# Kernel tuning notes

Hardware: AMD Instinct MI355X
Metric: run time of the kernel (lower is better)

## Reference

```python
import jax, jax.numpy as jnp
import numpy as np
from jax import lax

WEIGHT_REG = 1e-06
BIAS_REG = 1e-06
DROP_REG = 1e-05
EPS = 1e-07
TEMP = 0.1


def setup_inputs() -> dict:
    key = jax.random.key(0)
    ks = jax.random.split(key, 9)
    B, T, D, H = 256, 512, 128, 128
    x = jax.random.normal(ks[0], (B, T, D), dtype=jnp.float32)
    # 0.05 scale keeps LSTM gates out of deep saturation
    weight_ih = jax.random.normal(ks[1], (4 * H, D), dtype=jnp.float32) * 0.05
    weight_hh = jax.random.normal(ks[2], (4 * H, H), dtype=jnp.float32) * 0.05
    bias_ih = jax.random.normal(ks[3], (4 * H,), dtype=jnp.float32) * 0.05
    bias_hh = jax.random.normal(ks[4], (4 * H,), dtype=jnp.float32) * 0.05
    p_logit = jax.random.normal(ks[5], (1,), dtype=jnp.float32)
    p_logit_rec = jax.random.normal(ks[6], (1,), dtype=jnp.float32)
    unif_x = jax.random.uniform(ks[7], (B, D), dtype=jnp.float32)
    unif_h = jax.random.uniform(ks[8], (B, H), dtype=jnp.float32)
    return {"x": x, "weight_ih": weight_ih, "weight_hh": weight_hh,
            "bias_ih": bias_ih, "bias_hh": bias_hh,
            "p_logit": p_logit, "p_logit_rec": p_logit_rec,
            "unif_x": unif_x, "unif_h": unif_h}


def _concrete_mask(u, p):
    # random_tensor = 1 - sigmoid((logit(p) + logit(u)) / temp)
    logit = (jnp.log(p + EPS) - jnp.log(1.0 - p + EPS)
             + jnp.log(u + EPS) - jnp.log(1.0 - u + EPS))
    return 1.0 - jax.nn.sigmoid(logit / TEMP)


def reference(x, weight_ih, weight_hh, bias_ih, bias_hh,
              p_logit, p_logit_rec, unif_x, unif_h):
    B, T, D = x.shape
    H = weight_hh.shape[1]
    p = jax.nn.sigmoid(p_logit)        # [1]
    p_rec = jax.nn.sigmoid(p_logit_rec)  # [1]

    # masks are sampled once (at t=0) and reused every timestep
    mask_x = _concrete_mask(unif_x, p)      # [B, D]
    mask_h = _concrete_mask(unif_h, p_rec)  # [B, H]

    x_d = x * mask_x[:, None, :] / (1.0 - p)  # dropout on input, all steps

    h0 = jnp.zeros((B, H), dtype=x.dtype)
    c0 = jnp.zeros((B, H), dtype=x.dtype)

    def step(carry, xt):
        h, c = carry
        hd = h * mask_h / (1.0 - p_rec)  # recurrent concrete dropout
        gates = xt @ weight_ih.T + bias_ih + hd @ weight_hh.T + bias_hh
        i_g, f_g, g_g, o_g = jnp.split(gates, 4, axis=-1)  # torch LSTMCell order
        c_new = jax.nn.sigmoid(f_g) * c + jax.nn.sigmoid(i_g) * jnp.tanh(g_g)
        h_new = jax.nn.sigmoid(o_g) * jnp.tanh(c_new)
        return (h_new, c_new), h_new

    (h_last, _), hs = lax.scan(step, (h0, c0), jnp.swapaxes(x_d, 0, 1))
    x_out = jnp.swapaxes(hs, 0, 1)  # [B, T, H]

    sum_kernel = jnp.sum(weight_ih ** 2)
    sum_rec = jnp.sum(weight_hh ** 2)
    sum_bias = jnp.sum(bias_ih ** 2) + jnp.sum(bias_hh ** 2)
    weights_reg = WEIGHT_REG * (sum_kernel / (1.0 - p) + sum_rec / (1.0 - p_rec))
    bias_reg = BIAS_REG * sum_bias
    ent_k = p * jnp.log(p) + (1.0 - p) * jnp.log(1.0 - p)
    ent_r = p_rec * jnp.log(p_rec) + (1.0 - p_rec) * jnp.log(1.0 - p_rec)
    drop_reg = DROP_REG * (D * ent_k + H * ent_r)
    regularization = weights_reg + bias_reg + drop_reg  # [1]

    return (x_out, h_last, regularization, p, p_rec)
```

## Files before the change

### kernel.cpp

```cpp
#include <hip/hip_runtime.h>
#include <cstddef>

#define NB 256
#define NT 512
#define ND 128
#define NH 128
#define NG 512
#define NM (NB * NT)

constexpr float F_EPS  = 1e-7f;
constexpr float F_TEMP = 0.1f;

typedef _Float16 h2_t __attribute__((ext_vector_type(2)));
typedef _Float16 h4_t __attribute__((ext_vector_type(4)));
typedef _Float16 h8_t __attribute__((ext_vector_type(8)));
typedef float    fx4  __attribute__((ext_vector_type(4)));

#if defined(__has_builtin)
#  if __has_builtin(__builtin_amdgcn_fdot2)
#    define FDOT2(a, b, c) __builtin_amdgcn_fdot2((a), (b), (c), false)
#  endif
#endif
#ifndef FDOT2
#  define FDOT2(a, b, c) ((c) + (float)(a)[0] * (float)(b)[0] + (float)(a)[1] * (float)(b)[1])
#endif

__device__ __forceinline__ float fexp2(float x) {
#if defined(__has_builtin)
#  if __has_builtin(__builtin_amdgcn_exp2f)
    return __builtin_amdgcn_exp2f(x);
#  else
    return exp2f(x);
#  endif
#else
    return exp2f(x);
#endif
}
__device__ __forceinline__ float frcp(float x) {
#if defined(__has_builtin)
#  if __has_builtin(__builtin_amdgcn_rcpf)
    return __builtin_amdgcn_rcpf(x);
#  else
    return 1.0f / x;
#  endif
#else
    return 1.0f / x;
#endif
}
__device__ __forceinline__ float fsig(float x) {
    return frcp(1.0f + fexp2(x * -1.44269504088896f));
}
__device__ __forceinline__ float ftanh(float x) {
    return 1.0f - 2.0f * frcp(1.0f + fexp2(x * 2.88539008177793f));
}
__device__ __forceinline__ float sig(float x) { return 1.0f / (1.0f + expf(-x)); }

__device__ __forceinline__ void bar_lds() {
    asm volatile("s_waitcnt lgkmcnt(0)" ::: "memory");
    __builtin_amdgcn_sched_barrier(0);
    __builtin_amdgcn_s_barrier();
}

__global__ __launch_bounds__(256) void k_convert(const float* __restrict__ wih,
        const float* __restrict__ whh, _Float16* __restrict__ wih_h,
        _Float16* __restrict__ whh_h, float* __restrict__ partial) {
    int i = blockIdx.x * 256 + threadIdx.x;
    float4 a = ((const float4*)wih)[i];
    float4 b = ((const float4*)whh)[i];
    h4_t ah, bh;
    ah[0] = (_Float16)a.x; ah[1] = (_Float16)a.y; ah[2] = (_Float16)a.z; ah[3] = (_Float16)a.w;
    bh[0] = (_Float16)b.x; bh[1] = (_Float16)b.y; bh[2] = (_Float16)b.z; bh[3] = (_Float16)b.w;
    *(h4_t*)(wih_h + 4 * (size_t)i) = ah;
    *(h4_t*)(whh_h + 4 * (size_t)i) = bh;
    float sk = a.x * a.x + a.y * a.y + a.z * a.z + a.w * a.w;
    float sr = b.x * b.x + b.y * b.y + b.z * b.z + b.w * b.w;
    for (int off = 32; off; off >>= 1) {
        sk += __shfl_down(sk, off);
        sr += __shfl_down(sr, off);
    }
    if ((threadIdx.x & 63) == 0) {
        atomicAdd(partial + 0, sk);
        atomicAdd(partial + 1, sr);
    }
}

__global__ void k_tail(const float* __restrict__ bih, const float* __restrict__ bhh,
                       const float* __restrict__ pl, const float* __restrict__ plr,
                       const float* __restrict__ partial, float* __restrict__ out_tail) {
    __shared__ float red[8];
    int t = threadIdx.x;
    float v = bih[t], w2 = bhh[t];
    float sb = v * v + w2 * w2;
    for (int off = 32; off; off >>= 1) sb += __shfl_down(sb, off);
    int wid = t >> 6, lane = t & 63;
    if (lane == 0) red[wid] = sb;
    __syncthreads();
    if (t == 0) {
        float SB = 0.f;
        for (int i = 0; i < 8; i++) SB += red[i];
        float SK = partial[0], SR = partial[1];
        float p  = sig(pl[0]);
        float pr = sig(plr[0]);
        float wr = 1e-6f * (SK / (1.f - p) + SR / (1.f - pr));
        float br = 1e-6f * SB;
        float ek = p * logf(p) + (1.f - p) * logf(1.f - p);
        float er = pr * logf(pr) + (1.f - pr) * logf(1.f - pr);
        float dr = 1e-5f * ((float)ND * ek + (float)NH * er);
        out_tail[0] = wr + br + dr;
        out_tail[1] = p;
        out_tail[2] = pr;
    }
}

__global__ __launch_bounds__(256, 2) void k_gemm(const float* __restrict__ x,
        const _Float16* __restrict__ wih_h, const float* __restrict__ bih,
        const float* __restrict__ bhh, const float* __restrict__ pl,
        const float* __restrict__ unif_x, _Float16* __restrict__ Gp) {
    __shared__ _Float16 Alds[128 * 128];
    __shared__ _Float16 Wlds[128 * 128];
    __shared__ float sx[128];
    __shared__ float bsum[128];
    int t  = threadIdx.x;
    int m0 = blockIdx.x * 128;
    int j0 = blockIdx.y * 128;
    int b  = m0 >> 9;

    float p = sig(pl[0]);
    if (t < 128) {
        float u  = unif_x[b * ND + t];
        float lg = logf(p + F_EPS) - logf(1.f - p + F_EPS)
                 + logf(u + F_EPS) - logf(1.f - u + F_EPS);
        float mk = 1.f - sig(lg / F_TEMP);
        sx[t] = mk / (1.f - p);
    } else {
        int j = t - 128;
        bsum[j] = bih[j0 + j] + bhh[j0 + j];
    }
    __syncthreads();

#pragma unroll
    for (int i = 0; i < 8; i++) {
        int s   = i * 256 + t;
        int row = s >> 4;
        int s16 = s & 15;
        const float4* xp = (const float4*)(x + (size_t)(m0 + row) * ND + s16 * 8);
        float4 v0 = xp[0], v1 = xp[1];
        float4 s0 = *(const float4*)(sx + s16 * 8);
        float4 s1 = *(const float4*)(sx + s16 * 8 + 4);
        h8_t hv;
        hv[0] = (_Float16)(v0.x * s0.x); hv[1] = (_Float16)(v0.y * s0.y);
        hv[2] = (_Float16)(v0.z * s0.z); hv[3] = (_Float16)(v0.w * s0.w);
        hv[4] = (_Float16)(v1.x * s1.x); hv[5] = (_Float16)(v1.y * s1.y);
        hv[6] = (_Float16)(v1.z * s1.z); hv[7] = (_Float16)(v1.w * s1.w);
        *(h8_t*)(&Alds[(size_t)row * 128 + ((s16 ^ (row & 7)) << 3)]) = hv;
        h8_t wv = *(const h8_t*)(wih_h + (size_t)(j0 + row) * ND + s16 * 8);
        *(h8_t*)(&Wlds[(size_t)row * 128 + ((s16 ^ (row & 7)) << 3)]) = wv;
    }
    __syncthreads();

    int w  = t >> 6, l = t & 63;
    int lr = l & 15, lg = l >> 4;
    fx4 acc[2][8] = {};
#pragma unroll
    for (int kk = 0; kk < 4; kk++) {
        h8_t af[2], bf[8];
#pragma unroll
        for (int mt = 0; mt < 2; mt++) {
            int r = 32 * w + 16 * mt + lr;
            af[mt] = *(const h8_t*)(&Alds[(size_t)r * 128 + (((4 * kk + lg) ^ (r & 7)) << 3)]);
        }
#pragma unroll
        for (int nt = 0; nt < 8; nt++) {
            int r = 16 * nt + lr;
            bf[nt] = *(const h8_t*)(&Wlds[(size_t)r * 128 + (((4 * kk + lg) ^ (r & 7)) << 3)]);
        }
#pragma unroll
        for (int mt = 0; mt < 2; mt++)
#pragma unroll
            for (int nt = 0; nt < 8; nt++)
                acc[mt][nt] = __builtin_amdgcn_mfma_f32_16x16x32_f16(af[mt], bf[nt], acc[mt][nt], 0, 0, 0);
    }

#pragma unroll
    for (int mt = 0; mt < 2; mt++)
#pragma unroll
        for (int nt = 0; nt < 8; nt++) {
            int j = j0 + 16 * nt + lr;
            int m = m0 + 32 * w + 16 * mt + 4 * lg;
            float bv = bsum[16 * nt + lr];
            h4_t o;
#pragma unroll
            for (int q = 0; q < 4; q++) o[q] = (_Float16)(acc[mt][nt][q] + bv);
            *(h4_t*)(Gp + (size_t)j * NM + m) = o;
        }
}

__global__ __launch_bounds__(512, 2) void k_lstm(const _Float16* __restrict__ Gp,
        const _Float16* __restrict__ whh_h, const float* __restrict__ plr,
        const float* __restrict__ unif_h,
        float* __restrict__ xout, float* __restrict__ hlast) {
    __shared__ _Float16 hd[128];
    __shared__ float gates[512];
    int b = blockIdx.x;
    int j = threadIdx.x;
    int gate = j >> 7;

    h2_t w[64];
    {
        const _Float16* wr = whh_h + (size_t)j * NH;
#pragma unroll
        for (int i = 0; i < 16; i++) {
            h8_t a = *(const h8_t*)(wr + 8 * i);
#pragma unroll
            for (int q = 0; q < 4; q++)
                w[4 * i + q] = (h2_t){a[2 * q], a[2 * q + 1]};
        }
    }

    float pr = sig(plr[0]);
    float h = 0.f, c = 0.f, msk = 0.f;
    if (j < 128) {
        float u  = unif_h[b * NH + j];
        float lg = logf(pr + F_EPS) - logf(1.f - pr + F_EPS)
                 + logf(u + F_EPS) - logf(1.f - u + F_EPS);
        float mk = 1.f - sig(lg / F_TEMP);
        msk = mk / (1.f - pr);
        hd[j] = (_Float16)0.f;
    }

    const _Float16* gp = Gp + (size_t)j * NM + (size_t)b * NT;
    float* xo = xout + (size_t)b * NT * NH + j;

    h8_t gcur = *(const h8_t*)(gp);
    __syncthreads();

    for (int w8 = 0; w8 < NT / 8; w8++) {
        h8_t gnx = gcur;
        if (w8 + 1 < NT / 8) gnx = *(const h8_t*)(gp + 8 * (w8 + 1));
#pragma unroll
        for (int e = 0; e < 8; e++) {
            float a0 = 0.f, a1 = 0.f, a2 = 0.f, a3 = 0.f;
#pragma unroll
            for (int i = 0; i < 16; i++) {
                h8_t hv = *(const h8_t*)(&hd[8 * i]);
                a0 = FDOT2(((h2_t){hv[0], hv[1]}), w[4 * i + 0], a0);
                a1 = FDOT2(((h2_t){hv[2], hv[3]}), w[4 * i + 1], a1);
                a2 = FDOT2(((h2_t){hv[4], hv[5]}), w[4 * i + 2], a2);
                a3 = FDOT2(((h2_t){hv[6], hv[7]}), w[4 * i + 3], a3);
            }
            float s = (float)gcur[e] + ((a0 + a1) + (a2 + a3));
            gates[j] = (gate == 2) ? ftanh(s) : fsig(s);
            bar_lds();
            if (j < 128) {
                float ig = gates[j],       fg = gates[j + 128];
                float gg = gates[j + 256], og = gates[j + 384];
                c = fg * c + ig * gg;
                h = og * ftanh(c);
                hd[j] = (_Float16)(h * msk);
                xo[(size_t)(8 * w8 + e) * NH] = h;
            }
            bar_lds();
        }
        gcur = gnx;
    }
    if (j < 128) hlast[(size_t)b * NH + j] = h;
}

extern "C" void kernel_launch(void* const* d_in, const int* in_sizes, int n_in,
                              void* d_out, int out_size, void* d_ws, size_t ws_size,
                              hipStream_t stream) {
    const float* x   = (const float*)d_in[0];
    const float* wih = (const float*)d_in[1];
    const float* whh = (const float*)d_in[2];
    const float* bih = (const float*)d_in[3];
    const float* bhh = (const float*)d_in[4];
    const float* pl  = (const float*)d_in[5];
    const float* plr = (const float*)d_in[6];
    const float* ux  = (const float*)d_in[7];
    const float* uh  = (const float*)d_in[8];

    float* out   = (float*)d_out;
    float* xout  = out;
    float* hlast = out + (size_t)NB * NT * NH;
    float* tail  = hlast + (size_t)NB * NH;

    _Float16* G     = (_Float16*)d_ws;
    _Float16* wih_h = (_Float16*)((char*)d_ws + (size_t)NG * NM * 2);
    _Float16* whh_h = wih_h + (size_t)NG * ND;
    float*    partial = (float*)(whh_h + (size_t)NG * NH);

    hipMemsetAsync(partial, 0, 2 * sizeof(float), stream);

    k_convert<<<64, 256, 0, stream>>>(wih, whh, wih_h, whh_h, partial);

    dim3 gg(NM / 128, NG / 128);
    k_gemm<<<gg, 256, 0, stream>>>(x, wih_h, bih, bhh, pl, ux, G);

    k_tail<<<1, 512, 0, stream>>>(bih, bhh, pl, plr, partial, tail);

    k_lstm<<<NB, 512, 0, stream>>>(G, whh_h, plr, uh, xout, hlast);
}
```

Before: 372.5 us.

## Split LSTM recurrent dot product across two thread halves per gate

New measurement: 393.7 us. +5.7%, slower.

```diff
diff --git a/kernel.cpp b/kernel.cpp
--- a/kernel.cpp
+++ b/kernel.cpp
@@ -195,21 +195,22 @@
         }
 }
 
-__global__ __launch_bounds__(512, 2) void k_lstm(const _Float16* __restrict__ Gp,
+__global__ __launch_bounds__(1024, 4) void k_lstm(const _Float16* __restrict__ Gp,
         const _Float16* __restrict__ whh_h, const float* __restrict__ plr,
         const float* __restrict__ unif_h,
         float* __restrict__ xout, float* __restrict__ hlast) {
     __shared__ _Float16 hd[128];
-    __shared__ float gates[512];
-    int b = blockIdx.x;
-    int j = threadIdx.x;
-    int gate = j >> 7;
-
-    h2_t w[64];
+    __shared__ float part[1024];
+    int b    = blockIdx.x;
+    int tid  = threadIdx.x;
+    int j    = tid & 511;
+    int half = tid >> 9;
+
+    h2_t w[32];
     {
-        const _Float16* wr = whh_h + (size_t)j * NH;
-#pragma unroll
-        for (int i = 0; i < 16; i++) {
+        const _Float16* wr = whh_h + (size_t)j * NH + 64 * half;
+#pragma unroll
+        for (int i = 0; i < 8; i++) {
             h8_t a = *(const h8_t*)(wr + 8 * i);
 #pragma unroll
             for (int q = 0; q < 4; q++)
@@ -219,51 +220,61 @@
 
     float pr = sig(plr[0]);
     float h = 0.f, c = 0.f, msk = 0.f;
-    if (j < 128) {
-        float u  = unif_h[b * NH + j];
+    if (tid < 128) {
+        float u  = unif_h[b * NH + tid];
         float lg = logf(pr + F_EPS) - logf(1.f - pr + F_EPS)
                  + logf(u + F_EPS) - logf(1.f - u + F_EPS);
         float mk = 1.f - sig(lg / F_TEMP);
         msk = mk / (1.f - pr);
-        hd[j] = (_Float16)0.f;
+        hd[tid] = (_Float16)0.f;
     }
 
     const _Float16* gp = Gp + (size_t)j * NM + (size_t)b * NT;
-    float* xo = xout + (size_t)b * NT * NH + j;
-
-    h8_t gcur = *(const h8_t*)(gp);
+    float* xo = xout + (size_t)b * NT * NH + tid;
+
+    h8_t gcur;
+#pragma unroll
+    for (int e = 0; e < 8; e++) gcur[e] = (_Float16)0.f;
+    if (half == 0) gcur = *(const h8_t*)(gp);
     __syncthreads();
 
     for (int w8 = 0; w8 < NT / 8; w8++) {
+#pragma unroll
+        for (int i = 0; i < 32; i++) asm volatile("" : "+v"(w[i]));
         h8_t gnx = gcur;
-        if (w8 + 1 < NT / 8) gnx = *(const h8_t*)(gp + 8 * (w8 + 1));
+        if (half == 0 && w8 + 1 < NT / 8)
+            gnx = *(const h8_t*)(gp + 8 * (w8 + 1));
+        const _Float16* hb = &hd[64 * half];
 #pragma unroll
         for (int e = 0; e < 8; e++) {
             float a0 = 0.f, a1 = 0.f, a2 = 0.f, a3 = 0.f;
 #pragma unroll
-            for (int i = 0; i < 16; i++) {
-                h8_t hv = *(const h8_t*)(&hd[8 * i]);
+            for (int i = 0; i < 8; i++) {
+                h8_t hv = *(const h8_t*)(hb + 8 * i);
                 a0 = FDOT2(((h2_t){hv[0], hv[1]}), w[4 * i + 0], a0);
                 a1 = FDOT2(((h2_t){hv[2], hv[3]}), w[4 * i + 1], a1);
                 a2 = FDOT2(((h2_t){hv[4], hv[5]}), w[4 * i + 2], a2);
                 a3 = FDOT2(((h2_t){hv[6], hv[7]}), w[4 * i + 3], a3);
             }
-            float s = (float)gcur[e] + ((a0 + a1) + (a2 + a3));
-            gates[j] = (gate == 2) ? ftanh(s) : fsig(s);
+            part[tid] = (float)gcur[e] + ((a0 + a1) + (a2 + a3));
             bar_lds();
-            if (j < 128) {
-                float ig = gates[j],       fg = gates[j + 128];
-                float gg = gates[j + 256], og = gates[j + 384];
+            if (tid < 128) {
+                float si = part[tid]       + part[tid + 512];
+                float sf = part[tid + 128] + part[tid + 640];
+                float sg = part[tid + 256] + part[tid + 768];
+                float so = part[tid + 384] + part[tid + 896];
+                float ig = fsig(si), fg = fsig(sf);
+                float gg = ftanh(sg), og = fsig(so);
                 c = fg * c + ig * gg;
                 h = og * ftanh(c);
-                hd[j] = (_Float16)(h * msk);
+                hd[tid] = (_Float16)(h * msk);
                 xo[(size_t)(8 * w8 + e) * NH] = h;
             }
             bar_lds();
         }
         gcur = gnx;
     }
-    if (j < 128) hlast[(size_t)b * NH + j] = h;
+    if (tid < 128) hlast[(size_t)b * NH + tid] = h;
 }
 
 extern "C" void kernel_launch(void* const* d_in, const int* in_sizes, int n_in,
@@ -298,5 +309,5 @@
 
     k_tail<<<1, 512, 0, stream>>>(bih, bhh, pl, plr, partial, tail);
 
-    k_lstm<<<NB, 512, 0, stream>>>(G, whh_h, plr, uh, xout, hlast);
-}
+    k_lstm<<<NB, 1024, 0, stream>>>(G, whh_h, plr, uh, xout, hlast);
+}
```

## Exchange LSTM gates via wave shuffles with double-buffered hidden state, one barrier

Applied to the files above, without the earlier changes.

Result: slower. 419.6 us (+12.6%).

```diff
diff --git a/kernel.cpp b/kernel.cpp
--- a/kernel.cpp
+++ b/kernel.cpp
@@ -7,6 +7,7 @@
 #define NH 128
 #define NG 512
 #define NM (NB * NT)
+#define NMP (NM + 64)
 
 constexpr float F_EPS  = 1e-7f;
 constexpr float F_TEMP = 0.1f;
@@ -47,11 +48,8 @@
     return 1.0f / x;
 #endif
 }
-__device__ __forceinline__ float fsig(float x) {
-    return frcp(1.0f + fexp2(x * -1.44269504088896f));
-}
 __device__ __forceinline__ float ftanh(float x) {
-    return 1.0f - 2.0f * frcp(1.0f + fexp2(x * 2.88539008177793f));
+    return 1.0f - 2.0f * frcp(1.0f + fexp2(x * 2.885390081777927f));
 }
 __device__ __forceinline__ float sig(float x) { return 1.0f / (1.0f + expf(-x)); }
 
@@ -191,19 +189,22 @@
             h4_t o;
 #pragma unroll
             for (int q = 0; q < 4; q++) o[q] = (_Float16)(acc[mt][nt][q] + bv);
-            *(h4_t*)(Gp + (size_t)j * NM + m) = o;
-        }
-}
-
-__global__ __launch_bounds__(512, 2) void k_lstm(const _Float16* __restrict__ Gp,
+            *(h4_t*)(Gp + (size_t)j * NMP + m) = o;
+        }
+}
+
+__global__ __launch_bounds__(512, 1) void k_lstm(const _Float16* __restrict__ Gp,
         const _Float16* __restrict__ whh_h, const float* __restrict__ plr,
         const float* __restrict__ unif_h,
         float* __restrict__ xout, float* __restrict__ hlast) {
-    __shared__ _Float16 hd[128];
-    __shared__ float gates[512];
-    int b = blockIdx.x;
-    int j = threadIdx.x;
-    int gate = j >> 7;
+    __shared__ _Float16 hd[2][128];
+    int b   = blockIdx.x;
+    int tid = threadIdx.x;
+    int l   = tid & 63;
+    int wv  = tid >> 6;
+    int n   = wv * 16 + (l & 15);
+    int g   = (l >> 4) & 3;
+    int j   = g * 128 + n;
 
     h2_t w[64];
     {
@@ -218,52 +219,65 @@
     }
 
     float pr = sig(plr[0]);
-    float h = 0.f, c = 0.f, msk = 0.f;
-    if (j < 128) {
-        float u  = unif_h[b * NH + j];
+    float msk;
+    {
+        float u  = unif_h[b * NH + n];
         float lg = logf(pr + F_EPS) - logf(1.f - pr + F_EPS)
                  + logf(u + F_EPS) - logf(1.f - u + F_EPS);
         float mk = 1.f - sig(lg / F_TEMP);
         msk = mk / (1.f - pr);
-        hd[j] = (_Float16)0.f;
-    }
-
-    const _Float16* gp = Gp + (size_t)j * NM + (size_t)b * NT;
-    float* xo = xout + (size_t)b * NT * NH + j;
+    }
+    float h = 0.f, c = 0.f;
+    if (g == 0) hd[0][n] = (_Float16)0.f;
+
+    const float k1 = (g == 2) ?  2.885390081777927f : -1.44269504088896f;
+    const float Ac = (g == 2) ? -2.f : 1.f;
+    const float Bc = (g == 2) ?  1.f : 0.f;
+
+    const _Float16* gp = Gp + (size_t)j * NMP + (size_t)b * NT;
+    float* xo = xout + (size_t)b * NT * NH + n;
 
     h8_t gcur = *(const h8_t*)(gp);
     __syncthreads();
 
     for (int w8 = 0; w8 < NT / 8; w8++) {
+#pragma unroll
+        for (int i = 0; i < 64; i++) asm volatile("" : "+v"(w[i]));
         h8_t gnx = gcur;
-        if (w8 + 1 < NT / 8) gnx = *(const h8_t*)(gp + 8 * (w8 + 1));
+        if (w8 + 1 < NT / 8)
+            gnx = *(const h8_t*)(gp + 8 * (w8 + 1));
 #pragma unroll
         for (int e = 0; e < 8; e++) {
+            const _Float16* hb = &hd[e & 1][0];
             float a0 = 0.f, a1 = 0.f, a2 = 0.f, a3 = 0.f;
 #pragma unroll
             for (int i = 0; i < 16; i++) {
-                h8_t hv = *(const h8_t*)(&hd[8 * i]);
+                h8_t hv = *(const h8_t*)(hb + 8 * i);
                 a0 = FDOT2(((h2_t){hv[0], hv[1]}), w[4 * i + 0], a0);
                 a1 = FDOT2(((h2_t){hv[2], hv[3]}), w[4 * i + 1], a1);
                 a2 = FDOT2(((h2_t){hv[4], hv[5]}), w[4 * i + 2], a2);
                 a3 = FDOT2(((h2_t){hv[6], hv[7]}), w[4 * i + 3], a3);
             }
-            float s = (float)gcur[e] + ((a0 + a1) + (a2 + a3));
-            gates[j] = (gate == 2) ? ftanh(s) : fsig(s);
-            bar_lds();
-            if (j < 128) {
-                float ig = gates[j],       fg = gates[j + 128];
-                float gg = gates[j + 256], og = gates[j + 384];
-                c = fg * c + ig * gg;
-                h = og * ftanh(c);
-                hd[j] = (_Float16)(h * msk);
+            float s   = (float)gcur[e] + ((a0 + a1) + (a2 + a3));
+            float act = Bc + Ac * frcp(1.f + fexp2(s * k1));
+            float r1 = __shfl_xor(act, 16, 64);
+            float r2 = __shfl_xor(act, 32, 64);
+            float r3 = __shfl_xor(r1, 32, 64);
+            float iv = (g == 0) ? act : (g == 1) ? r1 : (g == 2) ? r2 : r3;
+            float fv = (g == 1) ? act : (g == 0) ? r1 : (g == 3) ? r2 : r3;
+            float gv = (g == 2) ? act : (g == 3) ? r1 : (g == 0) ? r2 : r3;
+            float ov = (g == 3) ? act : (g == 2) ? r1 : (g == 1) ? r2 : r3;
+            c = fv * c + iv * gv;
+            h = ov * ftanh(c);
+            if (g == 0) {
+                hd[(e & 1) ^ 1][n] = (_Float16)(h * msk);
                 xo[(size_t)(8 * w8 + e) * NH] = h;
             }
             bar_lds();
         }
         gcur = gnx;
     }
-    if (j < 128) hlast[(size_t)b * NH + j] = h;
+    if (g == 0) hlast[(size_t)b * NH + n] = h;
 }
 
 extern "C" void kernel_launch(void* const* d_in, const int* in_sizes, int n_in,
@@ -285,7 +299,7 @@
     float* tail  = hlast + (size_t)NB * NH;
 
     _Float16* G     = (_Float16*)d_ws;
-    _Float16* wih_h = (_Float16*)((char*)d_ws + (size_t)NG * NM * 2);
+    _Float16* wih_h = (_Float16*)((char*)d_ws + (size_t)NG * NMP * 2);
     _Float16* whh_h = wih_h + (size_t)NG * ND;
     float*    partial = (float*)(whh_h + (size_t)NG * NH);
 
```

## Batch sixteen sequences per LSTM block and compute recurrent gates with MFMA

Applied to the files above, without the earlier changes.

Result: slower. 748.6 us (+101.0%).

```diff
diff --git a/kernel.cpp b/kernel.cpp
--- a/kernel.cpp
+++ b/kernel.cpp
@@ -7,23 +7,15 @@
 #define NH 128
 #define NG 512
 #define NM (NB * NT)
+#define NMP (NM + 64)
+#define LBLK 16
 
 constexpr float F_EPS  = 1e-7f;
 constexpr float F_TEMP = 0.1f;
 
-typedef _Float16 h2_t __attribute__((ext_vector_type(2)));
 typedef _Float16 h4_t __attribute__((ext_vector_type(4)));
 typedef _Float16 h8_t __attribute__((ext_vector_type(8)));
 typedef float    fx4  __attribute__((ext_vector_type(4)));
-
-#if defined(__has_builtin)
-#  if __has_builtin(__builtin_amdgcn_fdot2)
-#    define FDOT2(a, b, c) __builtin_amdgcn_fdot2((a), (b), (c), false)
-#  endif
-#endif
-#ifndef FDOT2
-#  define FDOT2(a, b, c) ((c) + (float)(a)[0] * (float)(b)[0] + (float)(a)[1] * (float)(b)[1])
-#endif
 
 __device__ __forceinline__ float fexp2(float x) {
 #if defined(__has_builtin)
@@ -51,7 +43,7 @@
     return frcp(1.0f + fexp2(x * -1.44269504088896f));
 }
 __device__ __forceinline__ float ftanh(float x) {
-    return 1.0f - 2.0f * frcp(1.0f + fexp2(x * 2.88539008177793f));
+    return 1.0f - 2.0f * frcp(1.0f + fexp2(x * 2.885390081777927f));
 }
 __device__ __forceinline__ float sig(float x) { return 1.0f / (1.0f + expf(-x)); }
 
@@ -62,8 +54,11 @@
 }
 
 __global__ __launch_bounds__(256) void k_convert(const float* __restrict__ wih,
-        const float* __restrict__ whh, _Float16* __restrict__ wih_h,
-        _Float16* __restrict__ whh_h, float* __restrict__ partial) {
+        const float* __restrict__ whh, const float* __restrict__ pl,
+        const float* __restrict__ plr, const float* __restrict__ unif_x,
+        const float* __restrict__ unif_h, _Float16* __restrict__ wih_h,
+        _Float16* __restrict__ whh_h, _Float16* __restrict__ mask_x,
+        _Float16* __restrict__ mask_h, float* __restrict__ partial) {
     int i = blockIdx.x * 256 + threadIdx.x;
     float4 a = ((const float4*)wih)[i];
     float4 b = ((const float4*)whh)[i];
@@ -82,6 +77,26 @@
         atomicAdd(partial + 0, sk);
         atomicAdd(partial + 1, sr);
     }
+    float p;
+    const float* up;
+    _Float16* mp;
+    int mi;
+    if (i < 8192) { p = sig(pl[0]);  up = unif_x; mp = mask_x; mi = i; }
+    else          { p = sig(plr[0]); up = unif_h; mp = mask_h; mi = i - 8192; }
+    float4 u = ((const float4*)up)[mi];
+    float base = logf(p + F_EPS) - logf(1.f - p + F_EPS);
+    float inv  = 1.f / (1.f - p);
+    h4_t m4;
+    {
+        float uu[4] = {u.x, u.y, u.z, u.w};
+#pragma unroll
+        for (int e = 0; e < 4; ++e) {
+            float lg = base + logf(uu[e] + F_EPS) - logf(1.f - uu[e] + F_EPS);
+            float mk = 1.f - sig(lg / F_TEMP);
+            m4[e] = (_Float16)(mk * inv);
+        }
+    }
+    *(h4_t*)(mp + 4 * (size_t)mi) = m4;
 }
 
 __global__ void k_tail(const float* __restrict__ bih, const float* __restrict__ bhh,
@@ -114,28 +129,18 @@
 
 __global__ __launch_bounds__(256, 2) void k_gemm(const float* __restrict__ x,
         const _Float16* __restrict__ wih_h, const float* __restrict__ bih,
-        const float* __restrict__ bhh, const float* __restrict__ pl,
-        const float* __restrict__ unif_x, _Float16* __restrict__ Gp) {
+        const float* __restrict__ bhh, const _Float16* __restrict__ mask_x,
+        _Float16* __restrict__ Gp) {
     __shared__ _Float16 Alds[128 * 128];
     __shared__ _Float16 Wlds[128 * 128];
-    __shared__ float sx[128];
     __shared__ float bsum[128];
     int t  = threadIdx.x;
     int m0 = blockIdx.x * 128;
     int j0 = blockIdx.y * 128;
-    int b  = m0 >> 9;
-
-    float p = sig(pl[0]);
-    if (t < 128) {
-        float u  = unif_x[b * ND + t];
-        float lg = logf(p + F_EPS) - logf(1.f - p + F_EPS)
-                 + logf(u + F_EPS) - logf(1.f - u + F_EPS);
-        float mk = 1.f - sig(lg / F_TEMP);
-        sx[t] = mk / (1.f - p);
-    } else {
-        int j = t - 128;
-        bsum[j] = bih[j0 + j] + bhh[j0 + j];
-    }
+    int tg  = blockIdx.x >> 1;
+    int b0g = (blockIdx.x & 1) * 128;
+
+    if (t < 128) bsum[t] = bih[j0 + t] + bhh[j0 + t];
     __syncthreads();
 
 #pragma unroll
@@ -143,15 +148,15 @@
         int s   = i * 256 + t;
         int row = s >> 4;
         int s16 = s & 15;
-        const float4* xp = (const float4*)(x + (size_t)(m0 + row) * ND + s16 * 8);
+        int bb  = b0g + row;
+        const float4* xp = (const float4*)(x + ((size_t)bb * NT + tg) * ND + s16 * 8);
         float4 v0 = xp[0], v1 = xp[1];
-        float4 s0 = *(const float4*)(sx + s16 * 8);
-        float4 s1 = *(const float4*)(sx + s16 * 8 + 4);
+        h8_t mk = *(const h8_t*)(mask_x + (size_t)bb * ND + s16 * 8);
         h8_t hv;
-        hv[0] = (_Float16)(v0.x * s0.x); hv[1] = (_Float16)(v0.y * s0.y);
-        hv[2] = (_Float16)(v0.z * s0.z); hv[3] = (_Float16)(v0.w * s0.w);
-        hv[4] = (_Float16)(v1.x * s1.x); hv[5] = (_Float16)(v1.y * s1.y);
-        hv[6] = (_Float16)(v1.z * s1.z); hv[7] = (_Float16)(v1.w * s1.w);
+        hv[0] = (_Float16)(v0.x * (float)mk[0]); hv[1] = (_Float16)(v0.y * (float)mk[1]);
+        hv[2] = (_Float16)(v0.z * (float)mk[2]); hv[3] = (_Float16)(v0.w * (float)mk[3]);
+        hv[4] = (_Float16)(v1.x * (float)mk[4]); hv[5] = (_Float16)(v1.y * (float)mk[5]);
+        hv[6] = (_Float16)(v1.z * (float)mk[6]); hv[7] = (_Float16)(v1.w * (float)mk[7]);
         *(h8_t*)(&Alds[(size_t)row * 128 + ((s16 ^ (row & 7)) << 3)]) = hv;
         h8_t wv = *(const h8_t*)(wih_h + (size_t)(j0 + row) * ND + s16 * 8);
         *(h8_t*)(&Wlds[(size_t)row * 128 + ((s16 ^ (row & 7)) << 3)]) = wv;
@@ -191,79 +196,109 @@
             h4_t o;
 #pragma unroll
             for (int q = 0; q < 4; q++) o[q] = (_Float16)(acc[mt][nt][q] + bv);
-            *(h4_t*)(Gp + (size_t)j * NM + m) = o;
-        }
-}
-
-__global__ __launch_bounds__(512, 2) void k_lstm(const _Float16* __restrict__ Gp,
-        const _Float16* __restrict__ whh_h, const float* __restrict__ plr,
-        const float* __restrict__ unif_h,
-        float* __restrict__ xout, float* __restrict__ hlast) {
-    __shared__ _Float16 hd[128];
-    __shared__ float gates[512];
-    int b = blockIdx.x;
-    int j = threadIdx.x;
-    int gate = j >> 7;
-
-    h2_t w[64];
+            *(h4_t*)(Gp + (size_t)j * NMP + m) = o;
+        }
+}
+
+__global__ __launch_bounds__(512, 1)
+void k_lstm(const _Float16* __restrict__ Gp, const _Float16* __restrict__ whh_h,
+            const _Float16* __restrict__ maskh,
+            float* __restrict__ xout, float* __restrict__ hlast) {
+    __shared__ _Float16 hd[2][LBLK * 128];
+    int tid = threadIdx.x;
+    int l   = tid & 63;
+    int wv  = tid >> 6;
+    int lr  = l & 15;
+    int lq  = l >> 4;
+    int bc  = ((blockIdx.x & 7) << 1) | (blockIdx.x >> 3);
+    int b0  = bc * LBLK;
+    int u   = wv * 16 + lr;
+
+    h8_t bf[4][4];
+#pragma unroll
+    for (int g = 0; g < 4; ++g)
+#pragma unroll
+        for (int kk = 0; kk < 4; ++kk)
+            bf[g][kk] = *(const h8_t*)(whh_h + (size_t)(g * 128 + u) * NH + kk * 32 + lq * 8);
+
+    float msk[4], c4[4], hl[4];
+#pragma unroll
+    for (int r = 0; r < 4; ++r) {
+        msk[r] = (float)maskh[(size_t)(b0 + lq * 4 + r) * NH + u];
+        c4[r] = 0.f; hl[r] = 0.f;
+    }
+
+    const _Float16* gp0 = Gp + (size_t)(0 * 128 + u) * NMP + b0 + lq * 4;
+    const _Float16* gp1 = Gp + (size_t)(1 * 128 + u) * NMP + b0 + lq * 4;
+    const _Float16* gp2 = Gp + (size_t)(2 * 128 + u) * NMP + b0 + lq * 4;
+    const _Float16* gp3 = Gp + (size_t)(3 * 128 + u) * NMP + b0 + lq * 4;
+    float* xo0 = xout + (size_t)(b0 + lq * 4 + 0) * NT * NH + u;
+    float* xo1 = xout + (size_t)(b0 + lq * 4 + 1) * NT * NH + u;
+    float* xo2 = xout + (size_t)(b0 + lq * 4 + 2) * NT * NH + u;
+    float* xo3 = xout + (size_t)(b0 + lq * 4 + 3) * NT * NH + u;
+
     {
-        const _Float16* wr = whh_h + (size_t)j * NH;
-#pragma unroll
-        for (int i = 0; i < 16; i++) {
-            h8_t a = *(const h8_t*)(wr + 8 * i);
-#pragma unroll
-            for (int q = 0; q < 4; q++)
-                w[4 * i + q] = (h2_t){a[2 * q], a[2 * q + 1]};
-        }
-    }
-
-    float pr = sig(plr[0]);
-    float h = 0.f, c = 0.f, msk = 0.f;
-    if (j < 128) {
-        float u  = unif_h[b * NH + j];
-        float lg = logf(pr + F_EPS) - logf(1.f - pr + F_EPS)
-                 + logf(u + F_EPS) - logf(1.f - u + F_EPS);
-        float mk = 1.f - sig(lg / F_TEMP);
-        msk = mk / (1.f - pr);
-        hd[j] = (_Float16)0.f;
-    }
-
-    const _Float16* gp = Gp + (size_t)j * NM + (size_t)b * NT;
-    float* xo = xout + (size_t)b * NT * NH + j;
-
-    h8_t gcur = *(const h8_t*)(gp);
+        char* h0 = (char*)&hd[0][0];
+#pragma unroll
+        for (int r = 0; r < 4; ++r) {
+            int m = lq * 4 + r;
+            *(_Float16*)(h0 + m * 256 + ((2 * u) ^ ((m & 7) << 4))) = (_Float16)0.f;
+        }
+    }
     __syncthreads();
 
-    for (int w8 = 0; w8 < NT / 8; w8++) {
-        h8_t gnx = gcur;
-        if (w8 + 1 < NT / 8) gnx = *(const h8_t*)(gp + 8 * (w8 + 1));
-#pragma unroll
-        for (int e = 0; e < 8; e++) {
-            float a0 = 0.f, a1 = 0.f, a2 = 0.f, a3 = 0.f;
-#pragma unroll
-            for (int i = 0; i < 16; i++) {
-                h8_t hv = *(const h8_t*)(&hd[8 * i]);
-                a0 = FDOT2(((h2_t){hv[0], hv[1]}), w[4 * i + 0], a0);
-                a1 = FDOT2(((h2_t){hv[2], hv[3]}), w[4 * i + 1], a1);
-                a2 = FDOT2(((h2_t){hv[4], hv[5]}), w[4 * i + 2], a2);
-                a3 = FDOT2(((h2_t){hv[6], hv[7]}), w[4 * i + 3], a3);
-            }
-            float s = (float)gcur[e] + ((a0 + a1) + (a2 + a3));
-            gates[j] = (gate == 2) ? ftanh(s) : fsig(s);
-            bar_lds();
-            if (j < 128) {
-                float ig = gates[j],       fg = gates[j + 128];
-                float gg = gates[j + 256], og = gates[j + 384];
-                c = fg * c + ig * gg;
-                h = og * ftanh(c);
-                hd[j] = (_Float16)(h * msk);
-                xo[(size_t)(8 * w8 + e) * NH] = h;
-            }
-            bar_lds();
-        }
-        gcur = gnx;
-    }
-    if (j < 128) hlast[(size_t)b * NH + j] = h;
+    h4_t gA0 = *(const h4_t*)(gp0);
+    h4_t gA1 = *(const h4_t*)(gp1);
+    h4_t gA2 = *(const h4_t*)(gp2);
+    h4_t gA3 = *(const h4_t*)(gp3);
+
+    for (int t = 0; t < NT; ++t) {
+#pragma unroll
+        for (int g = 0; g < 4; ++g)
+#pragma unroll
+            for (int kk = 0; kk < 4; ++kk) asm volatile("" : "+v"(bf[g][kk]));
+        h4_t nA0 = gA0, nA1 = gA1, nA2 = gA2, nA3 = gA3;
+        if (t + 1 < NT) {
+            nA0 = *(const h4_t*)(gp0 + (size_t)(t + 1) * NB);
+            nA1 = *(const h4_t*)(gp1 + (size_t)(t + 1) * NB);
+            nA2 = *(const h4_t*)(gp2 + (size_t)(t + 1) * NB);
+            nA3 = *(const h4_t*)(gp3 + (size_t)(t + 1) * NB);
+        }
+        const char* hb = (const char*)&hd[t & 1][0];
+        fx4 a0 = {0.f, 0.f, 0.f, 0.f}, a1 = a0, a2 = a0, a3 = a0;
+#pragma unroll
+        for (int kk = 0; kk < 4; ++kk) {
+            h8_t af = *(const h8_t*)(hb + lr * 256 + ((kk * 64 + lq * 16) ^ ((lr & 7) << 4)));
+            a0 = __builtin_amdgcn_mfma_f32_16x16x32_f16(af, bf[0][kk], a0, 0, 0, 0);
+            a1 = __builtin_amdgcn_mfma_f32_16x16x32_f16(af, bf[1][kk], a1, 0, 0, 0);
+            a2 = __builtin_amdgcn_mfma_f32_16x16x32_f16(af, bf[2][kk], a2, 0, 0, 0);
+            a3 = __builtin_amdgcn_mfma_f32_16x16x32_f16(af, bf[3][kk], a3, 0, 0, 0);
+        }
+        char* hw = (char*)&hd[(t & 1) ^ 1][0];
+#pragma unroll
+        for (int r = 0; r < 4; ++r) {
+            float si = a0[r] + (float)gA0[r];
+            float sf = a1[r] + (float)gA1[r];
+            float sg = a2[r] + (float)gA2[r];
+            float so = a3[r] + (float)gA3[r];
+            float iv = fsig(si), fv = fsig(sf);
+            float gv = ftanh(sg), ov = fsig(so);
+            c4[r] = fv * c4[r] + iv * gv;
+            float h = ov * ftanh(c4[r]);
+            hl[r] = h;
+            int m = lq * 4 + r;
+            *(_Float16*)(hw + m * 256 + ((2 * u) ^ ((m & 7) << 4))) = (_Float16)(h * msk[r]);
+        }
+        xo0[(size_t)t * NH] = hl[0];
+        xo1[(size_t)t * NH] = hl[1];
+        xo2[(size_t)t * NH] = hl[2];
+        xo3[(size_t)t * NH] = hl[3];
+        gA0 = nA0; gA1 = nA1; gA2 = nA2; gA3 = nA3;
+        bar_lds();
+    }
+#pragma unroll
+    for (int r = 0; r < 4; ++r)
+        hlast[(size_t)(b0 + lq * 4 + r) * NH + u] = hl[r];
 }
 
 extern "C" void kernel_launch(void* const* d_in, const int* in_sizes, int n_in,
@@ -284,19 +319,22 @@
     float* hlast = out + (size_t)NB * NT * NH;
     float* tail  = hlast + (size_t)NB * NH;
 
-    _Float16* G     = (_Float16*)d_ws;
-    _Float16* wih_h = (_Float16*)((char*)d_ws + (size_t)NG * NM * 2);
-    _Float16* whh_h = wih_h + (size_t)NG * ND;
-    float*    partial = (float*)(whh_h + (size_t)NG * NH);
+    _Float16* G      = (_Float16*)d_ws;
+    _Float16* wih_h  = G + (size_t)NG * NMP;
+    _Float16* whh_h  = wih_h + (size_t)NG * ND;
+    _Float16* mask_x = whh_h + (size_t)NG * NH;
+    _Float16* mask_h = mask_x + (size_t)NB * ND;
+    float*    partial = (float*)(mask_h + (size_t)NB * NH);
 
     hipMemsetAsync(partial, 0, 2 * sizeof(float), stream);
 
-    k_convert<<<64, 256, 0, stream>>>(wih, whh, wih_h, whh_h, partial);
+    k_convert<<<64, 256, 0, stream>>>(wih, whh, pl, plr, ux, uh,
+                                      wih_h, whh_h, mask_x, mask_h, partial);
 
     dim3 gg(NM / 128, NG / 128);
-    k_gemm<<<gg, 256, 0, stream>>>(x, wih_h, bih, bhh, pl, ux, G);
+    k_gemm<<<gg, 256, 0, stream>>>(x, wih_h, bih, bhh, mask_x, G);
 
     k_tail<<<1, 512, 0, stream>>>(bih, bhh, pl, plr, partial, tail);
 
-    k_lstm<<<NB, 512, 0, stream>>>(G, whh_h, plr, uh, xout, hlast);
-}
+    k_lstm<<<NB / LBLK, 512, 0, stream>>>(G, whh_h, mask_h, xout, hlast);
+}
```
